# Kernel tuning notes

Measured on AMD Instinct MI355X. Metric: run time of the kernel, lower is better.

The kernel has to match this reference:

```python
import jax, jax.numpy as jnp
import numpy as np
from jax import lax

N_VAR, BATCH, N_IN, N_OUT, N_FEAT, T = 4, 32, 32, 32, 32, 256
EPS, COUPLING, GMAX, GMIN = 0.05, 0.2, 10.0, 0.01
DT, RMIN, RMAX, CMIN, CMAX = 0.1, 1e5, 1e7, 1e-7, 1e-4
ETA = np.array([0.05, 0.5, 0.3, 3.0], dtype=np.float32)  # printed-tanh activation params


def _init_theta(key, n_in, n_out):
    # xavier_uniform -> min-max normalize to [0,1], then bias-column construction as in pLayer.__init__
    a = float(np.sqrt(6.0 / (n_in + 2 + n_out)))
    t = jax.random.uniform(key, (n_in + 2, n_out), minval=-a, maxval=a)
    t = (t - t.min()) / (t.max() - t.min())
    t = t.at[-1, :].add(GMAX)
    t = t.at[-2, :].set(ETA[2] / (1.0 - ETA[2]) * (t[:-2].sum(0) + t[-1]))
    return t.astype(jnp.float32)


def setup_inputs():
    key = jax.random.key(0)
    kx, k1, k2 = jax.random.split(key, 3)
    x = jax.random.uniform(kx, (N_VAR, BATCH, N_IN, T), dtype=jnp.float32)
    theta1_ = _init_theta(k1, N_IN, N_OUT)
    theta2_ = _init_theta(k2, N_OUT * (N_FEAT + 1), N_OUT)
    # LearnableFilter init from beta_init (C_ fixed at -10, R_ is logit of normalized R)
    betas = np.linspace(0.1, 0.9, N_OUT)
    b0 = betas[:N_FEAT]
    b1 = betas[::-1][:N_FEAT]
    C_mean = 1.0 / (1.0 + np.exp(10.0)) * (CMAX - CMIN) + CMIN
    def r_(b):
        R_true = b * DT / (1.0 - b) / C_mean
        Rn = (R_true - RMIN) / (RMAX - RMIN)
        return np.log(Rn / (1.0 - Rn))
    Rlf_ = jnp.asarray(np.broadcast_to(np.stack([r_(b0), r_(b1)], -1), (N_OUT, N_FEAT, 2)).copy(), dtype=jnp.float32)
    Clf_ = jnp.full((N_OUT, N_FEAT, 2), -10.0, dtype=jnp.float32)
    return {"x": x, "theta1_": theta1_, "theta2_": theta2_, "Rlf_": Rlf_, "Clf_": Clf_}


def _theta_eff(theta_):
    # clamp + magnitude pruning with straight-through estimator
    t = jnp.clip(theta_, -GMAX, GMAX)
    t = jnp.where(jnp.abs(t) < GMIN, 0.0, t)
    return lax.stop_gradient(t) + theta_ - lax.stop_gradient(theta_)


def _pmac(a, theta_, key):
    # a: [N,B,Cin,T] -> [N,B,Cout,T]; printed MAC with sign-split weights and ideal inverter INV(a)=-a
    th = _theta_eff(theta_)
    noise = (jax.random.uniform(key, (N_VAR,) + th.shape) * 2.0 - 1.0) * EPS + 1.0
    thn = th[None] * noise  # [N,M,O]
    W = jnp.abs(thn) / (jnp.sum(jnp.abs(thn), axis=1, keepdims=True) + 1e-10)
    pos = (thn >= 0).astype(a.dtype)
    neg = 1.0 - pos
    ar = jnp.swapaxes(a, 2, 3)  # [N,B,T,Cin]
    ones = jnp.ones(ar.shape[:-1] + (1,), a.dtype)
    a_ext = jnp.concatenate([ar, ones, jnp.zeros_like(ones)], axis=-1)  # [N,B,T,M]
    a_neg = (-a_ext).at[..., -1].set(0.0)  # INV(a_ext) with last column zeroed
    z = jnp.einsum('nbtm,nmo->nbto', a_ext, W * pos) + jnp.einsum('nbtm,nmo->nbto', a_neg, W * neg)
    act = ETA[0] + ETA[1] * jnp.tanh((z - ETA[2]) * ETA[3])
    return jnp.swapaxes(act, 2, 3)


def _filter_bank(x, R_, C_, key):
    # x: [K,N,B,T]; first-order leaky integrator with fresh per-step R/C/mu noise, random init state
    K, N, B, Tt = x.shape
    Rt = jax.nn.sigmoid(R_) * (RMAX - RMIN) + RMIN  # [K]
    Ct = jax.nn.sigmoid(C_) * (CMAX - CMIN) + CMIN
    kR, kC, kmu, k0 = jax.random.split(key, 4)
    nR = (jax.random.uniform(kR, (Tt, K, N, 1)) * 2.0 - 1.0) * EPS + 1.0
    nC = (jax.random.uniform(kC, (Tt, K, N, 1)) * 2.0 - 1.0) * EPS + 1.0
    mu = jax.random.uniform(kmu, (Tt, K, N, 1)) * COUPLING + 1.0
    RC = mu * (Rt[None, :, None, None] * nR) * (Ct[None, :, None, None] * nC)
    beta = RC / (RC + DT)  # [T,K,N,1]
    s0 = jax.random.uniform(k0, (K, N, B))  # random_state=True
    xs = jnp.moveaxis(x, 3, 0)  # [T,K,N,B]
    def step(s, inp):
        x_t, b_t = inp
        return b_t * s + (1.0 - b_t) * x_t, s  # emit pre-update state (torch keeps init, drops last)
    _, outs = lax.scan(step, s0, (xs, beta))
    return jnp.moveaxis(outs, 0, 3)  # [K,N,B,T]


def reference(x, theta1_, theta2_, Rlf_, Clf_):
    key = jax.random.key(42)
    k1, k2, k3, k4 = jax.random.split(key, 4)
    a1 = _pmac(x, theta1_, k1)  # [N,B,C,T]
    N, B, C, Tt = a1.shape
    F = N_FEAT
    K = C * F
    xc = jnp.transpose(a1, (2, 0, 1, 3))  # [C,N,B,T]
    xk = jnp.broadcast_to(xc[:, None], (C, F, N, B, Tt)).reshape(K, N, B, Tt)
    y = _filter_bank(xk, Rlf_[..., 0].reshape(K), Clf_[..., 0].reshape(K), k2)
    y = _filter_bank(y, Rlf_[..., 1].reshape(K), Clf_[..., 1].reshape(K), k3)
    y = y.reshape(C, F, N, B, Tt)
    feats = jnp.concatenate([xc[:, None], y], axis=1)  # [C,F+1,N,B,T]
    h = jnp.transpose(feats, (2, 3, 0, 1, 4)).reshape(N, B, C * (F + 1), Tt)
    return _pmac(h, theta2_, k4)  # [N,B,N_out,T]
```

## Files before the change

### kernel.cpp

```cpp
#include <hip/hip_runtime.h>
#include <stdint.h>

#define C_RMIN 100000.0f
#define C_RMAX 10000000.0f
#define C_CMIN 1e-07f
#define C_CMAX 1e-04f
#define C_DT   0.1f
#define C_EPS  0.05f
#define C_COUP 0.2f

typedef __attribute__((ext_vector_type(8))) short bf16x8;
typedef __attribute__((ext_vector_type(4))) float floatx4;
union FragU { uint32_t u[4]; bf16x8 s; };

__host__ __device__ inline void tf2x32(uint32_t k0, uint32_t k1,
                                       uint32_t& x0, uint32_t& x1) {
  uint32_t ks2 = k0 ^ k1 ^ 0x1BD11BDAu;
  uint32_t a = x0 + k0, b = x1 + k1;
#define TFR(r) a += b; b = (b << (r)) | (b >> (32 - (r))); b ^= a;
  TFR(13) TFR(15) TFR(26) TFR(6)
  a += k1;  b += ks2 + 1u;
  TFR(17) TFR(29) TFR(16) TFR(24)
  a += ks2; b += k0 + 2u;
  TFR(13) TFR(15) TFR(26) TFR(6)
  a += k0;  b += k1 + 3u;
  TFR(17) TFR(29) TFR(16) TFR(24)
  a += k1;  b += ks2 + 4u;
  TFR(13) TFR(15) TFR(26) TFR(6)
  a += ks2; b += k0 + 5u;
#undef TFR
  x0 = a; x1 = b;
}

__device__ inline float unif01(uint32_t k0, uint32_t k1, uint32_t e) {
  uint32_t x0 = 0u, x1 = e;
  tf2x32(k0, k1, x0, x1);
  uint32_t bits = x0 ^ x1;
  return __uint_as_float((bits >> 9) | 0x3F800000u) - 1.0f;
}

__device__ inline float theta_eff(float t) {
  t = fminf(fmaxf(t, -10.0f), 10.0f);
  return (fabsf(t) < 0.01f) ? 0.0f : t;
}

__device__ inline float sigmoidf(float x) { return 1.0f / (1.0f + expf(-x)); }

__device__ inline float noise_mul(float u) { return (u * 2.0f - 1.0f) * C_EPS + 1.0f; }

__global__ __launch_bounds__(256) void prep0_kernel(
    const float* __restrict__ Rlf, const float* __restrict__ Clf,
    const float* __restrict__ theta1, const float* __restrict__ theta2,
    float* __restrict__ beta1, float* __restrict__ beta2,
    float* __restrict__ S1eff, float* __restrict__ denom2p,
    uint32_t k1a, uint32_t k1b, uint32_t k4a, uint32_t k4b,
    uint32_t kR1a, uint32_t kR1b, uint32_t kC1a, uint32_t kC1b,
    uint32_t kM1a, uint32_t kM1b,
    uint32_t kR2a, uint32_t kR2b, uint32_t kC2a, uint32_t kC2b,
    uint32_t kM2a, uint32_t kM2b) {
  int bid = blockIdx.x;
  if (bid < 32) {
    int n = bid >> 3, p = bid & 7;
    int o = threadIdx.x & 31;
    int jc = threadIdx.x >> 5;
    int j0 = p * 8 + jc;
    float part = 0.0f;
    for (int j = j0; j < 1058; j += 64) {
      float t = theta_eff(theta2[j * 32 + o]);
      float u = unif01(k4a, k4b, (uint32_t)((n * 1058 + j) * 32 + o));
      part += fabsf(t * noise_mul(u));
    }
    __shared__ float red[256];
    red[jc * 32 + o] = part;
    __syncthreads();
    if (jc == 0) {
      float s = 0.0f;
      for (int q = 0; q < 8; ++q) s += red[q * 32 + o];
      denom2p[(n * 8 + p) * 32 + o] = s;
    }
  } else if (bid < 36) {
    int n = bid - 32;
    int o = threadIdx.x;
    if (o < 32) {
      float tn[34];
      float den = 0.0f;
      for (int m = 0; m < 34; ++m) {
        float t = theta_eff(theta1[m * 32 + o]);
        float u = unif01(k1a, k1b, (uint32_t)((n * 34 + m) * 32 + o));
        float v = t * noise_mul(u);
        tn[m] = v;
        den += fabsf(v);
      }
      den += 1e-10f;
      for (int m = 0; m < 33; ++m)
        S1eff[(n * 33 + m) * 32 + o] = tn[m] / den;
    }
  } else {
    int u = (bid - 36) * 256 + threadIdx.x;
    int k = u & 1023;
    int tc = (u >> 10) & 31;
    int n = (u >> 15) & 3;
    int casc = u >> 17;
    uint32_t ra = casc ? kR2a : kR1a, rb = casc ? kR2b : kR1b;
    uint32_t ca = casc ? kC2a : kC1a, cb = casc ? kC2b : kC1b;
    uint32_t ma = casc ? kM2a : kM1a, mb = casc ? kM2b : kM1b;
    float R_ = Rlf[k * 2 + casc];
    float C_ = Clf[k * 2 + casc];
    float Rt = sigmoidf(R_) * (C_RMAX - C_RMIN) + C_RMIN;
    float Ct = sigmoidf(C_) * (C_CMAX - C_CMIN) + C_CMIN;
    float* outp = casc ? beta2 : beta1;
#pragma unroll
    for (int it = 0; it < 8; ++it) {
      int t = tc * 8 + it;
      uint32_t e = (uint32_t)((t * 1024 + k) * 4 + n);
      float nR = noise_mul(unif01(ra, rb, e));
      float nC = noise_mul(unif01(ca, cb, e));
      float mu = unif01(ma, mb, e) * C_COUP + 1.0f;
      float rc = mu * (Rt * nR) * (Ct * nC);
      outp[(n * 256 + t) * 1024 + k] = rc / (rc + C_DT);
    }
  }
}

__global__ __launch_bounds__(256) void prep1_kernel(
    const float* __restrict__ theta2, const float* __restrict__ denom2p,
    float* __restrict__ S2eff,
    const float* __restrict__ x, const float* __restrict__ S1eff,
    float* __restrict__ a1, uint32_t k4a, uint32_t k4b) {
  int bid = blockIdx.x;
  __shared__ float xs[32][256];
  if (bid < 128) {
    int n = bid >> 5, b = bid & 31;
    int t = threadIdx.x;
    const float* xp = x + (size_t)((n * 32 + b) * 32) * 256;
    for (int m = 0; m < 32; ++m) xs[m][t] = xp[m * 256 + t];
    __syncthreads();
    const float* S = S1eff + n * 33 * 32;
    float* ap = a1 + (size_t)((n * 32 + b) * 32) * 256;
    for (int o = 0; o < 32; ++o) {
      float z = S[32 * 32 + o];
#pragma unroll
      for (int m = 0; m < 32; ++m) z += xs[m][t] * S[m * 32 + o];
      ap[o * 256 + t] = 0.05f + 0.5f * tanhf((z - 0.3f) * 3.0f);
    }
  } else {
    int idx = (bid - 128) * 256 + threadIdx.x;
    if (idx >= 4 * 1057 * 32) return;
    int o = idx & 31;
    int r = idx >> 5;
    int j = r % 1057;
    int n = r / 1057;
    float den = 1e-10f;
#pragma unroll
    for (int p = 0; p < 8; ++p) den += denom2p[(n * 8 + p) * 32 + o];
    float t = theta_eff(theta2[j * 32 + o]);
    float u = unif01(k4a, k4b, (uint32_t)((n * 1058 + j) * 32 + o));
    S2eff[idx] = t * noise_mul(u) / den;
  }
}

#define YPAD 260
#define YBUF (16 * YPAD)

__global__ __launch_bounds__(320) void fk3_kernel(
    const float* __restrict__ a1, const float* __restrict__ S2eff,
    const float* __restrict__ beta1, const float* __restrict__ beta2,
    float* __restrict__ zpart,
    uint32_t k01a, uint32_t k01b, uint32_t k02a, uint32_t k02b) {
  int bid = blockIdx.x;
  int qr = bid & 3;
  int nb = bid >> 2;
  int n = nb >> 5, b = nb & 31;
  int tid = threadIdx.x;

  __shared__ __align__(16) uint32_t yb[2 * YBUF];
  __shared__ __align__(16) short wf[16 * 512];

  const float* S2n = S2eff + (size_t)n * 1057 * 32;
  const float* a1nb = a1 + (size_t)nb * 8192;
  const float* b1p = beta1 + (size_t)n * 262144 + qr * 256;
  const float* b2p = beta2 + (size_t)n * 262144 + qr * 256;
  float* zout = zpart + (size_t)bid * 8192;

  float s1 = 0.0f, s2 = 0.0f;
  int cc = 0;

  if (tid < 256) {
    int k = qr * 256 + tid;
    uint32_t e0 = (uint32_t)((k * 4 + n) * 32 + b);
    s1 = unif01(k01a, k01b, e0);
    s2 = unif01(k02a, k02b, e0);
    cc = k >> 5;
    for (int it = 0; it < 32; ++it) {
      int widx = it * 256 + tid;
      int j = widx & 7;
      int lane_ = (widx >> 3) & 63;
      int ot = (widx >> 9) & 1;
      int ks = widx >> 10;
      int sub = ((lane_ >> 4) << 3) + j;
      int jrow = (qr * 8 + ks) * 33 + 1 + sub;
      float w = S2n[jrow * 32 + ot * 16 + (lane_ & 15)];
      uint32_t wb = __float_as_uint(w);
      uint32_t hi = (wb + 0x7FFFu + ((wb >> 16) & 1u)) >> 16;
      wf[(ks * 2 + ot) * 512 + lane_ * 8 + j] = (short)(uint16_t)hi;
    }
  }
  __syncthreads();

  for (int c = 0; c <= 16; ++c) {
    if (tid < 256) {
      if (c < 16) {
        uint32_t* ybw = yb + (c & 1) * YBUF;
        int t0 = c * 16;
#pragma unroll
        for (int it = 0; it < 16; ++it) {
          int t = t0 + it;
          uint32_t sb = __float_as_uint(s2);
          uint32_t hi = sb >> 16;
          float fhi = __uint_as_float(sb & 0xFFFF0000u);
          uint32_t lo = __float_as_uint(s2 - fhi) >> 16;
          ybw[it * YPAD + tid] = (lo << 16) | hi;
          float bb1 = b1p[t * 1024 + tid];
          float bb2 = b2p[t * 1024 + tid];
          float xv = a1nb[cc * 256 + t];
          s2 = bb2 * s2 + (1.0f - bb2) * s1;
          s1 = bb1 * s1 + (1.0f - bb1) * xv;
        }
      }
    } else if (c >= 1) {
      const uint32_t* ybr = yb + ((c - 1) & 1) * YBUF;
      int lane = tid - 256;
      int tc = lane & 15, q = lane >> 4;
      const uint32_t* yrow = ybr + tc * YPAD + q * 8;
      floatx4 acc0a = {0,0,0,0}, acc0b = {0,0,0,0};
      floatx4 acc1a = {0,0,0,0}, acc1b = {0,0,0,0};
#pragma unroll
      for (int ks = 0; ks < 8; ++ks) {
        uint4 p0 = *(const uint4*)(yrow + ks * 32);
        uint4 p1 = *(const uint4*)(yrow + ks * 32 + 4);
        FragU ah, al;
        ah.u[0] = (p0.x & 0xFFFFu) | (p0.y << 16);
        ah.u[1] = (p0.z & 0xFFFFu) | (p0.w << 16);
        ah.u[2] = (p1.x & 0xFFFFu) | (p1.y << 16);
        ah.u[3] = (p1.z & 0xFFFFu) | (p1.w << 16);
        al.u[0] = (p0.x >> 16) | (p0.y & 0xFFFF0000u);
        al.u[1] = (p0.z >> 16) | (p0.w & 0xFFFF0000u);
        al.u[2] = (p1.x >> 16) | (p1.y & 0xFFFF0000u);
        al.u[3] = (p1.z >> 16) | (p1.w & 0xFFFF0000u);
        bf16x8 bh0 = *(const bf16x8*)&wf[(ks * 2 + 0) * 512 + lane * 8];
        bf16x8 bh1 = *(const bf16x8*)&wf[(ks * 2 + 1) * 512 + lane * 8];
        if (ks & 1) {
          acc0b = __builtin_amdgcn_mfma_f32_16x16x32_bf16(ah.s, bh0, acc0b, 0, 0, 0);
          acc0b = __builtin_amdgcn_mfma_f32_16x16x32_bf16(al.s, bh0, acc0b, 0, 0, 0);
          acc1b = __builtin_amdgcn_mfma_f32_16x16x32_bf16(ah.s, bh1, acc1b, 0, 0, 0);
          acc1b = __builtin_amdgcn_mfma_f32_16x16x32_bf16(al.s, bh1, acc1b, 0, 0, 0);
        } else {
          acc0a = __builtin_amdgcn_mfma_f32_16x16x32_bf16(ah.s, bh0, acc0a, 0, 0, 0);
          acc0a = __builtin_amdgcn_mfma_f32_16x16x32_bf16(al.s, bh0, acc0a, 0, 0, 0);
          acc1a = __builtin_amdgcn_mfma_f32_16x16x32_bf16(ah.s, bh1, acc1a, 0, 0, 0);
          acc1a = __builtin_amdgcn_mfma_f32_16x16x32_bf16(al.s, bh1, acc1a, 0, 0, 0);
        }
      }
      int t0 = (c - 1) * 16;
      floatx4 r0 = acc0a + acc0b;
      floatx4 r1 = acc1a + acc1b;
      *(floatx4*)&zout[tc * 256 + t0 + q * 4] = r0;
      *(floatx4*)&zout[(16 + tc) * 256 + t0 + q * 4] = r1;
    }
    __syncthreads();
  }
}

__global__ __launch_bounds__(256) void cb_kernel(
    const float* __restrict__ a1, const float* __restrict__ S2eff,
    const float* __restrict__ zpart, float* __restrict__ out) {
  int nb = blockIdx.x;
  int n = nb >> 5;
  int t = threadIdx.x;
  __shared__ float xs[32][256];
  const float* a1nb = a1 + (size_t)nb * 8192;
  for (int c = 0; c < 32; ++c) xs[c][t] = a1nb[c * 256 + t];
  __syncthreads();
  const float* S2n = S2eff + (size_t)n * 1057 * 32;
  const float* zp = zpart + (size_t)nb * 4 * 8192;
  float* op = out + (size_t)nb * 8192;
  for (int o = 0; o < 32; ++o) {
    float z = S2n[1056 * 32 + o];
#pragma unroll
    for (int c = 0; c < 32; ++c) z += xs[c][t] * S2n[(c * 33) * 32 + o];
    z += zp[o * 256 + t] + zp[8192 + o * 256 + t] +
         zp[16384 + o * 256 + t] + zp[24576 + o * 256 + t];
    op[o * 256 + t] = 0.05f + 0.5f * tanhf((z - 0.3f) * 3.0f);
  }
}

struct KeyPair { uint32_t a, b; };

static inline void split4_host(KeyPair key, KeyPair out[4]) {
  for (uint32_t i = 0; i < 4; ++i) {
    uint32_t x0 = 0u, x1 = i;
    tf2x32(key.a, key.b, x0, x1);
    out[i] = {x0, x1};
  }
}

extern "C" void kernel_launch(void* const* d_in, const int* in_sizes, int n_in,
                              void* d_out, int out_size, void* d_ws, size_t ws_size,
                              hipStream_t stream) {
  const float* x   = (const float*)d_in[0];
  const float* th1 = (const float*)d_in[1];
  const float* th2 = (const float*)d_in[2];
  const float* Rlf = (const float*)d_in[3];
  const float* Clf = (const float*)d_in[4];
  float* out = (float*)d_out;
  float* ws = (float*)d_ws;

  float* S1    = ws;
  float* den2p = ws + 4224;
  float* S2    = ws + 5248;
  float* a1    = ws + 140544;
  float* be1   = ws + 1189120;
  float* be2   = ws + 2237696;
  float* zpart = ws + 3286272;

  KeyPair root{0u, 42u};
  KeyPair kk[4];  split4_host(root, kk);
  KeyPair f1[4];  split4_host(kk[1], f1);
  KeyPair f2[4];  split4_host(kk[2], f2);

  prep0_kernel<<<dim3(1060), dim3(256), 0, stream>>>(
      Rlf, Clf, th1, th2, be1, be2, S1, den2p,
      kk[0].a, kk[0].b, kk[3].a, kk[3].b,
      f1[0].a, f1[0].b, f1[1].a, f1[1].b, f1[2].a, f1[2].b,
      f2[0].a, f2[0].b, f2[1].a, f2[1].b, f2[2].a, f2[2].b);
  prep1_kernel<<<dim3(657), dim3(256), 0, stream>>>(
      th2, den2p, S2, x, S1, a1, kk[3].a, kk[3].b);
  fk3_kernel<<<dim3(512), dim3(320), 0, stream>>>(
      a1, S2, be1, be2, zpart, f1[3].a, f1[3].b, f2[3].a, f2[3].b);
  cb_kernel<<<dim3(128), dim3(256), 0, stream>>>(a1, S2, zpart, out);
}
```

Before: 161.3 us.

## Interleave beta arrays, split y hi/lo planes, fuse final combine via last-block counter

The two filter-cascade beta arrays are merged into one interleaved float2 buffer, so prep0 computes both cascades per thread and the scan loads one float2 per step. The shared-memory y buffer is split into separate bf16 hi and lo planes, so the MFMA operands load directly without repacking. The separate combine kernel is removed: each fk block increments a per-(n,b) atomic counter, and the last of the four finishes the reduction and tanh. This saves a launch and repacking work, at the cost of a serialized tail inside the last block and the need to reset the counters on every call.

```diff
diff --git a/kernel.cpp b/kernel.cpp
--- a/kernel.cpp
+++ b/kernel.cpp
@@ -11,7 +11,6 @@
 
 typedef __attribute__((ext_vector_type(8))) short bf16x8;
 typedef __attribute__((ext_vector_type(4))) float floatx4;
-union FragU { uint32_t u[4]; bf16x8 s; };
 
 __host__ __device__ inline void tf2x32(uint32_t k0, uint32_t k1,
                                        uint32_t& x0, uint32_t& x1) {
@@ -51,8 +50,8 @@
 __global__ __launch_bounds__(256) void prep0_kernel(
     const float* __restrict__ Rlf, const float* __restrict__ Clf,
     const float* __restrict__ theta1, const float* __restrict__ theta2,
-    float* __restrict__ beta1, float* __restrict__ beta2,
-    float* __restrict__ S1eff, float* __restrict__ denom2p,
+    float* __restrict__ beta12, float* __restrict__ S1eff,
+    float* __restrict__ denom2p, int* __restrict__ cnt,
     uint32_t k1a, uint32_t k1b, uint32_t k4a, uint32_t k4b,
     uint32_t kR1a, uint32_t kR1b, uint32_t kC1a, uint32_t kC1b,
     uint32_t kM1a, uint32_t kM1b,
@@ -60,6 +59,7 @@
     uint32_t kM2a, uint32_t kM2b) {
   int bid = blockIdx.x;
   if (bid < 32) {
+    if (threadIdx.x < 4) cnt[bid * 4 + threadIdx.x] = 0;
     int n = bid >> 3, p = bid & 7;
     int o = threadIdx.x & 31;
     int jc = threadIdx.x >> 5;
@@ -99,25 +99,25 @@
     int u = (bid - 36) * 256 + threadIdx.x;
     int k = u & 1023;
     int tc = (u >> 10) & 31;
-    int n = (u >> 15) & 3;
-    int casc = u >> 17;
-    uint32_t ra = casc ? kR2a : kR1a, rb = casc ? kR2b : kR1b;
-    uint32_t ca = casc ? kC2a : kC1a, cb = casc ? kC2b : kC1b;
-    uint32_t ma = casc ? kM2a : kM1a, mb = casc ? kM2b : kM1b;
-    float R_ = Rlf[k * 2 + casc];
-    float C_ = Clf[k * 2 + casc];
-    float Rt = sigmoidf(R_) * (C_RMAX - C_RMIN) + C_RMIN;
-    float Ct = sigmoidf(C_) * (C_CMAX - C_CMIN) + C_CMIN;
-    float* outp = casc ? beta2 : beta1;
+    int n = u >> 15;
+    float Rt1 = sigmoidf(Rlf[k * 2 + 0]) * (C_RMAX - C_RMIN) + C_RMIN;
+    float Ct1 = sigmoidf(Clf[k * 2 + 0]) * (C_CMAX - C_CMIN) + C_CMIN;
+    float Rt2 = sigmoidf(Rlf[k * 2 + 1]) * (C_RMAX - C_RMIN) + C_RMIN;
+    float Ct2 = sigmoidf(Clf[k * 2 + 1]) * (C_CMAX - C_CMIN) + C_CMIN;
 #pragma unroll
     for (int it = 0; it < 8; ++it) {
       int t = tc * 8 + it;
       uint32_t e = (uint32_t)((t * 1024 + k) * 4 + n);
-      float nR = noise_mul(unif01(ra, rb, e));
-      float nC = noise_mul(unif01(ca, cb, e));
-      float mu = unif01(ma, mb, e) * C_COUP + 1.0f;
-      float rc = mu * (Rt * nR) * (Ct * nC);
-      outp[(n * 256 + t) * 1024 + k] = rc / (rc + C_DT);
+      float nR1 = noise_mul(unif01(kR1a, kR1b, e));
+      float nC1 = noise_mul(unif01(kC1a, kC1b, e));
+      float mu1 = unif01(kM1a, kM1b, e) * C_COUP + 1.0f;
+      float rc1 = mu1 * (Rt1 * nR1) * (Ct1 * nC1);
+      float nR2 = noise_mul(unif01(kR2a, kR2b, e));
+      float nC2 = noise_mul(unif01(kC2a, kC2b, e));
+      float mu2 = unif01(kM2a, kM2b, e) * C_COUP + 1.0f;
+      float rc2 = mu2 * (Rt2 * nR2) * (Ct2 * nC2);
+      float2 bb = { rc1 / (rc1 + C_DT), rc2 / (rc2 + C_DT) };
+      *(float2*)&beta12[(size_t)(((n * 256 + t) * 1024) + k) * 2] = bb;
     }
   }
 }
@@ -159,13 +159,13 @@
   }
 }
 
-#define YPAD 260
-#define YBUF (16 * YPAD)
-
-__global__ __launch_bounds__(320) void fk3_kernel(
+#define YP 264
+#define YPLANE (16 * YP)
+
+__global__ __launch_bounds__(320) void fk4_kernel(
     const float* __restrict__ a1, const float* __restrict__ S2eff,
-    const float* __restrict__ beta1, const float* __restrict__ beta2,
-    float* __restrict__ zpart,
+    const float* __restrict__ beta12, float* __restrict__ zpart,
+    float* __restrict__ out, int* __restrict__ cnt,
     uint32_t k01a, uint32_t k01b, uint32_t k02a, uint32_t k02b) {
   int bid = blockIdx.x;
   int qr = bid & 3;
@@ -173,13 +173,15 @@
   int n = nb >> 5, b = nb & 31;
   int tid = threadIdx.x;
 
-  __shared__ __align__(16) uint32_t yb[2 * YBUF];
-  __shared__ __align__(16) short wf[16 * 512];
+  __shared__ __align__(16) uint8_t smem[50176];
+  uint16_t* yh = (uint16_t*)smem;
+  uint16_t* yl = (uint16_t*)(smem + 16896);
+  short*    wf = (short*)(smem + 33792);
+  __shared__ int sflag;
 
   const float* S2n = S2eff + (size_t)n * 1057 * 32;
   const float* a1nb = a1 + (size_t)nb * 8192;
-  const float* b1p = beta1 + (size_t)n * 262144 + qr * 256;
-  const float* b2p = beta2 + (size_t)n * 262144 + qr * 256;
+  const float* bp = beta12 + ((size_t)n * 262144 + qr * 256) * 2;
   float* zout = zpart + (size_t)bid * 8192;
 
   float s1 = 0.0f, s2 = 0.0f;
@@ -210,7 +212,8 @@
   for (int c = 0; c <= 16; ++c) {
     if (tid < 256) {
       if (c < 16) {
-        uint32_t* ybw = yb + (c & 1) * YBUF;
+        uint16_t* yhb = yh + (c & 1) * YPLANE;
+        uint16_t* ylb = yl + (c & 1) * YPLANE;
         int t0 = c * 16;
 #pragma unroll
         for (int it = 0; it < 16; ++it) {
@@ -219,46 +222,37 @@
           uint32_t hi = sb >> 16;
           float fhi = __uint_as_float(sb & 0xFFFF0000u);
           uint32_t lo = __float_as_uint(s2 - fhi) >> 16;
-          ybw[it * YPAD + tid] = (lo << 16) | hi;
-          float bb1 = b1p[t * 1024 + tid];
-          float bb2 = b2p[t * 1024 + tid];
+          yhb[it * YP + tid] = (uint16_t)hi;
+          ylb[it * YP + tid] = (uint16_t)lo;
+          float2 bb = *(const float2*)&bp[(size_t)(t * 1024 + tid) * 2];
           float xv = a1nb[cc * 256 + t];
-          s2 = bb2 * s2 + (1.0f - bb2) * s1;
-          s1 = bb1 * s1 + (1.0f - bb1) * xv;
+          s2 = bb.y * s2 + (1.0f - bb.y) * s1;
+          s1 = bb.x * s1 + (1.0f - bb.x) * xv;
         }
       }
     } else if (c >= 1) {
-      const uint32_t* ybr = yb + ((c - 1) & 1) * YBUF;
       int lane = tid - 256;
       int tc = lane & 15, q = lane >> 4;
-      const uint32_t* yrow = ybr + tc * YPAD + q * 8;
+      const uint16_t* yhr = yh + ((c - 1) & 1) * YPLANE + tc * YP + q * 8;
+      const uint16_t* ylr = yl + ((c - 1) & 1) * YPLANE + tc * YP + q * 8;
       floatx4 acc0a = {0,0,0,0}, acc0b = {0,0,0,0};
       floatx4 acc1a = {0,0,0,0}, acc1b = {0,0,0,0};
 #pragma unroll
       for (int ks = 0; ks < 8; ++ks) {
-        uint4 p0 = *(const uint4*)(yrow + ks * 32);
-        uint4 p1 = *(const uint4*)(yrow + ks * 32 + 4);
-        FragU ah, al;
-        ah.u[0] = (p0.x & 0xFFFFu) | (p0.y << 16);
-        ah.u[1] = (p0.z & 0xFFFFu) | (p0.w << 16);
-        ah.u[2] = (p1.x & 0xFFFFu) | (p1.y << 16);
-        ah.u[3] = (p1.z & 0xFFFFu) | (p1.w << 16);
-        al.u[0] = (p0.x >> 16) | (p0.y & 0xFFFF0000u);
-        al.u[1] = (p0.z >> 16) | (p0.w & 0xFFFF0000u);
-        al.u[2] = (p1.x >> 16) | (p1.y & 0xFFFF0000u);
-        al.u[3] = (p1.z >> 16) | (p1.w & 0xFFFF0000u);
+        bf16x8 ah = *(const bf16x8*)(yhr + ks * 32);
+        bf16x8 al = *(const bf16x8*)(ylr + ks * 32);
         bf16x8 bh0 = *(const bf16x8*)&wf[(ks * 2 + 0) * 512 + lane * 8];
         bf16x8 bh1 = *(const bf16x8*)&wf[(ks * 2 + 1) * 512 + lane * 8];
         if (ks & 1) {
-          acc0b = __builtin_amdgcn_mfma_f32_16x16x32_bf16(ah.s, bh0, acc0b, 0, 0, 0);
-          acc0b = __builtin_amdgcn_mfma_f32_16x16x32_bf16(al.s, bh0, acc0b, 0, 0, 0);
-          acc1b = __builtin_amdgcn_mfma_f32_16x16x32_bf16(ah.s, bh1, acc1b, 0, 0, 0);
-          acc1b = __builtin_amdgcn_mfma_f32_16x16x32_bf16(al.s, bh1, acc1b, 0, 0, 0);
+          acc0b = __builtin_amdgcn_mfma_f32_16x16x32_bf16(ah, bh0, acc0b, 0, 0, 0);
+          acc0b = __builtin_amdgcn_mfma_f32_16x16x32_bf16(al, bh0, acc0b, 0, 0, 0);
+          acc1b = __builtin_amdgcn_mfma_f32_16x16x32_bf16(ah, bh1, acc1b, 0, 0, 0);
+          acc1b = __builtin_amdgcn_mfma_f32_16x16x32_bf16(al, bh1, acc1b, 0, 0, 0);
         } else {
-          acc0a = __builtin_amdgcn_mfma_f32_16x16x32_bf16(ah.s, bh0, acc0a, 0, 0, 0);
-          acc0a = __builtin_amdgcn_mfma_f32_16x16x32_bf16(al.s, bh0, acc0a, 0, 0, 0);
-          acc1a = __builtin_amdgcn_mfma_f32_16x16x32_bf16(ah.s, bh1, acc1a, 0, 0, 0);
-          acc1a = __builtin_amdgcn_mfma_f32_16x16x32_bf16(al.s, bh1, acc1a, 0, 0, 0);
+          acc0a = __builtin_amdgcn_mfma_f32_16x16x32_bf16(ah, bh0, acc0a, 0, 0, 0);
+          acc0a = __builtin_amdgcn_mfma_f32_16x16x32_bf16(al, bh0, acc0a, 0, 0, 0);
+          acc1a = __builtin_amdgcn_mfma_f32_16x16x32_bf16(ah, bh1, acc1a, 0, 0, 0);
+          acc1a = __builtin_amdgcn_mfma_f32_16x16x32_bf16(al, bh1, acc1a, 0, 0, 0);
         }
       }
       int t0 = (c - 1) * 16;
@@ -269,28 +263,32 @@
     }
     __syncthreads();
   }
-}
-
-__global__ __launch_bounds__(256) void cb_kernel(
-    const float* __restrict__ a1, const float* __restrict__ S2eff,
-    const float* __restrict__ zpart, float* __restrict__ out) {
-  int nb = blockIdx.x;
-  int n = nb >> 5;
-  int t = threadIdx.x;
-  __shared__ float xs[32][256];
-  const float* a1nb = a1 + (size_t)nb * 8192;
-  for (int c = 0; c < 32; ++c) xs[c][t] = a1nb[c * 256 + t];
+
+  if (tid == 0) {
+    __threadfence();
+    sflag = (atomicAdd(&cnt[nb], 1) == 3) ? 1 : 0;
+  }
   __syncthreads();
-  const float* S2n = S2eff + (size_t)n * 1057 * 32;
-  const float* zp = zpart + (size_t)nb * 4 * 8192;
-  float* op = out + (size_t)nb * 8192;
-  for (int o = 0; o < 32; ++o) {
-    float z = S2n[1056 * 32 + o];
-#pragma unroll
-    for (int c = 0; c < 32; ++c) z += xs[c][t] * S2n[(c * 33) * 32 + o];
-    z += zp[o * 256 + t] + zp[8192 + o * 256 + t] +
-         zp[16384 + o * 256 + t] + zp[24576 + o * 256 + t];
-    op[o * 256 + t] = 0.05f + 0.5f * tanhf((z - 0.3f) * 3.0f);
+  if (sflag == 0) return;
+  __threadfence();
+
+  float* xs = (float*)smem;
+  if (tid < 256) {
+    for (int c2 = 0; c2 < 32; ++c2) xs[c2 * 256 + tid] = a1nb[c2 * 256 + tid];
+  }
+  __syncthreads();
+  if (tid < 256) {
+    int t = tid;
+    const float* zp = zpart + (size_t)nb * 4 * 8192;
+    float* op = out + (size_t)nb * 8192;
+    for (int o = 0; o < 32; ++o) {
+      float z = S2n[1056 * 32 + o];
+#pragma unroll
+      for (int c2 = 0; c2 < 32; ++c2) z += xs[c2 * 256 + t] * S2n[(c2 * 33) * 32 + o];
+      z += zp[o * 256 + t] + zp[8192 + o * 256 + t] +
+           zp[16384 + o * 256 + t] + zp[24576 + o * 256 + t];
+      op[o * 256 + t] = 0.05f + 0.5f * tanhf((z - 0.3f) * 3.0f);
+    }
   }
 }
 
@@ -315,27 +313,26 @@
   float* out = (float*)d_out;
   float* ws = (float*)d_ws;
 
-  float* S1    = ws;
-  float* den2p = ws + 4224;
-  float* S2    = ws + 5248;
-  float* a1    = ws + 140544;
-  float* be1   = ws + 1189120;
-  float* be2   = ws + 2237696;
-  float* zpart = ws + 3286272;
+  float* S1     = ws;
+  float* den2p  = ws + 4224;
+  float* S2     = ws + 5248;
+  float* a1     = ws + 140544;
+  float* beta12 = ws + 1189120;
+  float* zpart  = ws + 3286272;
+  int*   cnt    = (int*)(ws + 7480576);
 
   KeyPair root{0u, 42u};
   KeyPair kk[4];  split4_host(root, kk);
   KeyPair f1[4];  split4_host(kk[1], f1);
   KeyPair f2[4];  split4_host(kk[2], f2);
 
-  prep0_kernel<<<dim3(1060), dim3(256), 0, stream>>>(
-      Rlf, Clf, th1, th2, be1, be2, S1, den2p,
+  prep0_kernel<<<dim3(548), dim3(256), 0, stream>>>(
+      Rlf, Clf, th1, th2, beta12, S1, den2p, cnt,
       kk[0].a, kk[0].b, kk[3].a, kk[3].b,
       f1[0].a, f1[0].b, f1[1].a, f1[1].b, f1[2].a, f1[2].b,
       f2[0].a, f2[0].b, f2[1].a, f2[1].b, f2[2].a, f2[2].b);
   prep1_kernel<<<dim3(657), dim3(256), 0, stream>>>(
       th2, den2p, S2, x, S1, a1, kk[3].a, kk[3].b);
-  fk3_kernel<<<dim3(512), dim3(320), 0, stream>>>(
-      a1, S2, be1, be2, zpart, f1[3].a, f1[3].b, f2[3].a, f2[3].b);
-  cb_kernel<<<dim3(128), dim3(256), 0, stream>>>(a1, S2, zpart, out);
-}
+  fk4_kernel<<<dim3(512), dim3(320), 0, stream>>>(
+      a1, S2, beta12, zpart, out, cnt, f1[3].a, f1[3].b, f2[3].a, f2[3].b);
+}
```

Measured after the change: 234.0 us. +45.1%, slower.
